# Optimization experiments

Hardware: AMD Instinct MI355X
Metric: run time of the kernel (lower is better)

The kernel has to match this reference:

```python
import jax, jax.numpy as jnp
import numpy as np

B, L, D = 32, 512, 256
MAX_DUR = 8


def setup_inputs() -> dict:
    key = jax.random.key(0)
    k1, k2 = jax.random.split(key)
    hidden_phonems = jax.random.normal(k1, (B, L, D), dtype=jnp.float32)
    durations = jax.random.randint(k2, (B, L), 0, MAX_DUR, dtype=jnp.int32)
    return {"hidden_phonems": hidden_phonems, "durations": durations}


def reference(hidden_phonems, durations):
    # hidden_phonems: [B, L, D], durations: [B, L] int
    totals = jnp.sum(durations, axis=1)                    # [B] mel length per utterance
    max_T = int(jnp.max(totals))                           # batch-max padded length (matches torch)
    cum = jnp.cumsum(durations, axis=1)                    # [B, L] exclusive-of-next prefix sums
    t = jnp.arange(max_T, dtype=jnp.int32)                 # output frame positions
    # frame t belongs to the first phoneme whose cumulative duration exceeds t
    idx = jax.vmap(lambda c: jnp.searchsorted(c, t, side='right'))(cum)  # [B, max_T]
    idx = jnp.clip(idx, 0, hidden_phonems.shape[1] - 1)
    out = jnp.take_along_axis(hidden_phonems, idx[:, :, None], axis=1)   # [B, max_T, D]
    mask = (t[None, :] < totals[:, None])                  # zero out padding frames
    return out * mask[:, :, None].astype(out.dtype)
```

## Files before the change

### kernel.cpp

```cpp
#include <hip/hip_runtime.h>

#define B_SZ 32
#define L_SZ 512
#define D_SZ 256
#define P_PER_WAVE 8
#define WAVES_TOTAL (B_SZ * L_SZ / P_PER_WAVE)
#define BLOCKS (WAVES_TOTAL / 4)

typedef float f4 __attribute__((ext_vector_type(4)));
typedef int   i4 __attribute__((ext_vector_type(4)));

__global__ void __launch_bounds__(256)
lr_kernel(const float* __restrict__ hidden,
          const int* __restrict__ durations,
          float* __restrict__ out,
          int maxT) {
    const int lane = threadIdx.x & 63;
    const int wv   = threadIdx.x >> 6;
    const int wid  = blockIdx.x * 4 + wv;
    const int b    = wid >> 6;
    const int g    = wid & 63;
    const int l0   = g * P_PER_WAVE;

    const f4* src = (const f4*)(hidden + ((size_t)(b * L_SZ + l0)) * D_SZ) + lane;
    f4 v[8];
    #pragma unroll
    for (int r = 0; r < 8; ++r) v[r] = __builtin_nontemporal_load(src + r * 64);

    const i4* drow = (const i4*)(durations + b * L_SZ);
    const i4 a = drow[lane * 2];
    const i4 c = drow[lane * 2 + 1];
    const int s = a.x + a.y + a.z + a.w + c.x + c.y + c.z + c.w;
    const int packed = a.x | (a.y << 3) | (a.z << 6) | (a.w << 9)
                     | (c.x << 12) | (c.y << 15) | (c.z << 18) | (c.w << 21);

    int p = ((lane < g) ? s : 0) + (s << 16);
    #pragma unroll
    for (int off = 32; off; off >>= 1) p += __shfl_xor(p, off, 64);
    int start       = p & 0xffff;
    const int total = ((unsigned)p) >> 16;

    const int pk = __shfl(packed, g, 64);

    float* obase = out + (size_t)b * maxT * D_SZ;
    #pragma unroll
    for (int r = 0; r < 8; ++r) {
        const int d = (pk >> (3 * r)) & 7;
        f4* dst = (f4*)(obase + (size_t)start * D_SZ) + lane;
        #pragma unroll
        for (int j = 0; j < 7; ++j)
            if (j < d) dst[j * 64] = v[r];
        start += d;
    }

    const f4 z = (f4){0.f, 0.f, 0.f, 0.f};
    for (int t = total + g; t < maxT; t += 64) {
        f4* dst = (f4*)(obase + (size_t)t * D_SZ) + lane;
        *dst = z;
    }
}

extern "C" void kernel_launch(void* const* d_in, const int* in_sizes, int n_in,
                              void* d_out, int out_size, void* d_ws, size_t ws_size,
                              hipStream_t stream) {
    const float* hidden = (const float*)d_in[0];
    const int* durations = (const int*)d_in[1];
    float* out = (float*)d_out;

    const int maxT = out_size / (B_SZ * D_SZ);

    lr_kernel<<<BLOCKS, 256, 0, stream>>>(hidden, durations, out, maxT);
}
```

Before: 83.78 us.

## Switch from scatter-per-phoneme to gather-per-output-frame parallelization

Each wave now owns 8 output frames instead of 8 input phonemes. It computes an inclusive scan of per-lane duration sums, finds the owning phoneme with a ballot and per-lane decode, then gathers the source row and writes it with nontemporal stores. Padding frames get zeros in the same pass. This removes the variable per-phoneme write count and the separate zero-fill loop, giving a uniform write pattern. In exchange, repeated phonemes are re-read from memory or cache, and each wave repeats the duration scan.

```diff
diff --git a/kernel.cpp b/kernel.cpp
--- a/kernel.cpp
+++ b/kernel.cpp
@@ -3,29 +3,24 @@
 #define B_SZ 32
 #define L_SZ 512
 #define D_SZ 256
-#define P_PER_WAVE 8
-#define WAVES_TOTAL (B_SZ * L_SZ / P_PER_WAVE)
-#define BLOCKS (WAVES_TOTAL / 4)
+#define FRAMES_PER_WAVE 8
+#define FRAMES_PER_BLOCK 32
 
 typedef float f4 __attribute__((ext_vector_type(4)));
 typedef int   i4 __attribute__((ext_vector_type(4)));
 
 __global__ void __launch_bounds__(256)
-lr_kernel(const float* __restrict__ hidden,
-          const int* __restrict__ durations,
-          float* __restrict__ out,
-          int maxT) {
-    const int lane = threadIdx.x & 63;
-    const int wv   = threadIdx.x >> 6;
-    const int wid  = blockIdx.x * 4 + wv;
-    const int b    = wid >> 6;
-    const int g    = wid & 63;
-    const int l0   = g * P_PER_WAVE;
-
-    const f4* src = (const f4*)(hidden + ((size_t)(b * L_SZ + l0)) * D_SZ) + lane;
-    f4 v[8];
-    #pragma unroll
-    for (int r = 0; r < 8; ++r) v[r] = __builtin_nontemporal_load(src + r * 64);
+lr_gather_kernel(const float* __restrict__ hidden,
+                 const int* __restrict__ durations,
+                 float* __restrict__ out,
+                 int maxT, int chunks) {
+    const int lane  = threadIdx.x & 63;
+    const int wv    = threadIdx.x >> 6;
+    const int bid   = blockIdx.x;
+    const int b     = bid / chunks;
+    const int chunk = bid - b * chunks;
+    const int t0    = chunk * FRAMES_PER_BLOCK + wv * FRAMES_PER_WAVE;
+    if (t0 >= maxT) return;
 
     const i4* drow = (const i4*)(durations + b * L_SZ);
     const i4 a = drow[lane * 2];
@@ -34,29 +29,38 @@
     const int packed = a.x | (a.y << 3) | (a.z << 6) | (a.w << 9)
                      | (c.x << 12) | (c.y << 15) | (c.z << 18) | (c.w << 21);
 
-    int p = ((lane < g) ? s : 0) + (s << 16);
+    int incl = s;
     #pragma unroll
-    for (int off = 32; off; off >>= 1) p += __shfl_xor(p, off, 64);
-    int start       = p & 0xffff;
-    const int total = ((unsigned)p) >> 16;
+    for (int off = 1; off < 64; off <<= 1) {
+        const int tt = __shfl_up(incl, off, 64);
+        if (lane >= off) incl += tt;
+    }
+    const int ex = incl - s;
 
-    const int pk = __shfl(packed, g, 64);
+    const float* hbase = hidden + (size_t)b * L_SZ * D_SZ;
+    float*       obase = out    + (size_t)b * maxT * D_SZ;
+    const f4 z = (f4){0.f, 0.f, 0.f, 0.f};
 
-    float* obase = out + (size_t)b * maxT * D_SZ;
     #pragma unroll
-    for (int r = 0; r < 8; ++r) {
-        const int d = (pk >> (3 * r)) & 7;
-        f4* dst = (f4*)(obase + (size_t)start * D_SZ) + lane;
-        #pragma unroll
-        for (int j = 0; j < 7; ++j)
-            if (j < d) dst[j * 64] = v[r];
-        start += d;
-    }
-
-    const f4 z = (f4){0.f, 0.f, 0.f, 0.f};
-    for (int t = total + g; t < maxT; t += 64) {
-        f4* dst = (f4*)(obase + (size_t)t * D_SZ) + lane;
-        *dst = z;
+    for (int f = 0; f < FRAMES_PER_WAVE; ++f) {
+        const int t = t0 + f;
+        if (t >= maxT) break;
+        const unsigned long long mask = __ballot(incl > t);
+        f4 v = z;
+        if (mask) {
+            const int l    = __ffsll(mask) - 1;
+            const int base = __shfl(ex, l, 64);
+            const int pk   = __shfl(packed, l, 64);
+            int acc = base, r = 0;
+            #pragma unroll
+            for (int k = 0; k < 7; ++k) {
+                acc += (pk >> (3 * k)) & 7;
+                r += (acc <= t);
+            }
+            const int row = l * 8 + r;
+            v = *((const f4*)(hbase + (size_t)row * D_SZ) + lane);
+        }
+        __builtin_nontemporal_store(v, (f4*)(obase + (size_t)t * D_SZ) + lane);
     }
 }
 
@@ -67,7 +71,9 @@
     const int* durations = (const int*)d_in[1];
     float* out = (float*)d_out;
 
-    const int maxT = out_size / (B_SZ * D_SZ);
+    const int maxT   = out_size / (B_SZ * D_SZ);
+    const int chunks = (maxT + FRAMES_PER_BLOCK - 1) / FRAMES_PER_BLOCK;
 
-    lr_kernel<<<BLOCKS, 256, 0, stream>>>(hidden, durations, out, maxT);
+    lr_gather_kernel<<<B_SZ * chunks, 256, 0, stream>>>(hidden, durations, out,
+                                                        maxT, chunks);
 }
```

After: 88.24 us, median of 2. 1.05x slower.
